# Kernel optimization log

Measured on AMD Instinct MI355X. Metric: run time of the kernel, lower is better.

## Reference

```python
import jax, jax.numpy as jnp
import numpy as np

BLOCKS = (1, 2, 3, 4)      # (block_size, offset=0) from max_block_size=4
BLOCK_MULT = 12            # lcm(1,2,3,4)
DS = 4                     # downsample_factor
MAX_BS = 4                 # max block size (also pos_conv kernel size)
DIM = 512
VOCAB = 256


def _masked_mean(t, m, axis):
    # t: [..., L, D], m: [..., L] bool -> mean over axis with mask, 0 where empty
    mf = m[..., None].astype(t.dtype)
    num = jnp.sum(t * mf, axis=axis)
    tot = jnp.sum(mf, axis=axis)
    mean = num / jnp.clip(tot, 1.0)
    return jnp.where(tot == 0.0, jnp.zeros_like(mean), mean)


def setup_inputs() -> dict:
    key = jax.random.key(0)
    ks = jax.random.split(key, 8)
    B, S = 8, 2048
    return {
        "x": jax.random.randint(ks[0], (B, S), 0, VOCAB),
        "mask": jnp.ones((B, S), dtype=bool),
        "emb": jax.random.normal(ks[1], (VOCAB, DIM), jnp.float32) * 0.02,
        "dw_w": jax.random.normal(ks[2], (MAX_BS, 1, DIM), jnp.float32) * 0.1,   # depthwise kernel (W, I=1, O=DIM)
        "dw_b": jnp.zeros((DIM,), jnp.float32),
        "pw_w": jax.random.normal(ks[3], (1, DIM, DIM), jnp.float32) * 0.03,     # pointwise 1x1 conv
        "pw_b": jnp.zeros((DIM,), jnp.float32),
        "score_w": jax.random.normal(ks[4], (DIM, 1), jnp.float32) * 0.05,
        "score_b": jnp.zeros((1,), jnp.float32),
    }


def reference(x, mask, emb, dw_w, dw_b, pw_w, pw_b, score_w, score_b):
    B, S = x.shape
    D = DIM
    trunc = ((S + DS - 1) // DS) * DS  # next_divisible_length(S, DS); equals S here

    h = emb[x]                                              # [B,S,D]
    h = jnp.pad(h, ((0, 0), (0, MAX_BS - 1), (0, 0)))       # right pad for VALID conv
    dn = jax.lax.conv_dimension_numbers(h.shape, dw_w.shape, ('NWC', 'WIO', 'NWC'))
    h = jax.lax.conv_general_dilated(h, dw_w, (1,), 'VALID',
                                     dimension_numbers=dn,
                                     feature_group_count=D) + dw_b  # depthwise -> [B,S,D]
    h = jnp.einsum('bsd,de->bse', h, pw_w[0]) + pw_b                # pointwise

    # pad seq to multiple of lcm of block sizes
    Sp = ((h.shape[1] + BLOCK_MULT - 1) // BLOCK_MULT) * BLOCK_MULT
    pad = Sp - h.shape[1]
    h = jnp.pad(h, ((0, 0), (0, pad), (0, 0)))
    m = jnp.pad(mask.astype(bool), ((0, 0), (0, pad)), constant_values=False)

    reprs, rmasks = [], []
    for bsz in BLOCKS:  # fixed small set of block sizes (offset=0 for all)
        nb = Sp // bsz
        g = h.reshape(B, nb, bsz, D)
        mg = m.reshape(B, nb, bsz)
        r = _masked_mean(g, mg, axis=2)                       # [B,nb,D]
        reprs.append(jnp.repeat(r, bsz, axis=1))              # [B,Sp,D]
        rmasks.append(jnp.repeat(jnp.any(mg, axis=-1), bsz, axis=1))

    block_reprs = jnp.stack(reprs, axis=2)    # [B,Sp,M,D]
    block_masks = jnp.stack(rmasks, axis=2)   # [B,Sp,M]

    scores = (block_reprs @ score_w)[..., 0] + score_b[0]     # [B,Sp,M]
    max_neg = -jnp.finfo(scores.dtype).max
    scores = jnp.where(block_masks, scores, max_neg)
    scores = jnp.nan_to_num(jax.nn.softmax(scores, axis=2), nan=0.0)

    # consensus attention over positions
    sim = jnp.einsum('bim,bjm->bij', scores, scores)          # [B,Sp,Sp]
    cm = m[:, :, None] & m[:, None, :]
    sim = jnp.where(cm, sim, max_neg)
    attn = jnp.nan_to_num(jax.nn.softmax(sim, axis=-1), nan=0.0)
    scores = jnp.einsum('bij,bjm->bim', attn, scores)

    out = jnp.einsum('bsmd,bsm->bsd', block_reprs, scores)    # weighted combine
    out = out[:, :trunc]
    mt = m[:, :trunc]

    nl = trunc // DS
    xb = out.reshape(B, nl, DS, D)
    mb = mt.reshape(B, nl, DS)
    out = _masked_mean(xb, mb, axis=2)                        # [B, S/DS, D]
    out_mask = jnp.any(mb, axis=-1)
    return out, out_mask
```

## Files before the change

### kernel.cpp

```cpp
#include <hip/hip_runtime.h>
#include <stdint.h>
#include <stddef.h>

typedef __bf16 bf16_t;
typedef bf16_t bf16x4v __attribute__((ext_vector_type(4)));
typedef bf16_t bf16x8v __attribute__((ext_vector_type(8)));
typedef float  f32x4   __attribute__((ext_vector_type(4)));

#define NBATCH 8
#define SEQ    2048
#define DIM    512
#define SP     2052
#define NL     512

static __device__ __forceinline__ f32x4 ldbf4(const bf16_t* p) {
  bf16x4v v = *(const bf16x4v*)p;
  f32x4 r;
  r.x = (float)v[0]; r.y = (float)v[1]; r.z = (float)v[2]; r.w = (float)v[3];
  return r;
}
static __device__ __forceinline__ void stbf4(bf16_t* p, f32x4 v) {
  bf16x4v o;
  o[0] = (bf16_t)v.x; o[1] = (bf16_t)v.y; o[2] = (bf16_t)v.z; o[3] = (bf16_t)v.w;
  *(bf16x4v*)p = o;
}

static __device__ __forceinline__ void gload_lds16(const void* g, void* l) {
  __builtin_amdgcn_global_load_lds(
      (const __attribute__((address_space(1))) void*)g,
      (__attribute__((address_space(3))) void*)l, 16, 0, 0);
}

#define GA_WT   256
#define GA_MASK 65
#define GA_A    (NBATCH * SEQ / 2)
__global__ __launch_bounds__(256) void kA_prep(
    const float* __restrict__ pw, bf16_t* __restrict__ Wt,
    const void* __restrict__ mraw, float* __restrict__ mask01,
    const int* __restrict__ x, const float* __restrict__ emb,
    const float* __restrict__ dww, const float* __restrict__ dwb,
    bf16_t* __restrict__ A) {
  const int bx = blockIdx.x, t = threadIdx.x;
  if (bx < GA_WT) {
    __shared__ float T[32][33];
    int ti = bx >> 4, tj = bx & 15;
    int r = t >> 3, c0 = (t & 7) * 4;
    f32x4 v = *(const f32x4*)(pw + (size_t)(ti * 32 + r) * DIM + tj * 32 + c0);
    T[c0 + 0][r] = v.x; T[c0 + 1][r] = v.y;
    T[c0 + 2][r] = v.z; T[c0 + 3][r] = v.w;
    __syncthreads();
    bf16x4v o;
    o[0] = (bf16_t)T[r][c0 + 0]; o[1] = (bf16_t)T[r][c0 + 1];
    o[2] = (bf16_t)T[r][c0 + 2]; o[3] = (bf16_t)T[r][c0 + 3];
    *(bf16x4v*)(Wt + (size_t)(tj * 32 + r) * DIM + ti * 32 + c0) = o;
    return;
  }
  if (bx < GA_WT + GA_MASK) {
    int idx = (bx - GA_WT) * 256 + t;
    if (idx >= NBATCH * SP) return;
    int b = idx / SP, s = idx - b * SP;
    const unsigned char* mb = (const unsigned char*)mraw;
    int u8 = 0;
#pragma unroll
    for (int i = 0; i < 64; i++)
      if ((i & 3) != 0 && mb[i] != 0) u8 = 1;
    float v = 0.f;
    if (s < SEQ) {
      int mi = b * SEQ + s;
      int nz = u8 ? (mb[mi] != 0) : (((const int*)mraw)[mi] != 0);
      v = nz ? 1.f : 0.f;
    }
    mask01[idx] = v;
    return;
  }
  int rp = bx - (GA_WT + GA_MASK);
  int row = rp * 2 + (t >> 7);
  int b = row >> 11, s = row & 2047;
  int d0 = (t & 127) * 4;
  f32x4 acc = *(const f32x4*)(dwb + d0);
#pragma unroll
  for (int tt = 0; tt < 4; tt++) {
    int sp = s + tt;
    if (sp < SEQ) {
      int v = x[b * SEQ + sp];
      f32x4 e = *(const f32x4*)(emb + (size_t)v * DIM + d0);
      f32x4 w = *(const f32x4*)(dww + tt * DIM + d0);
      acc += e * w;
    }
  }
  stbf4(A + (size_t)row * DIM + d0, acc);
}

#define BM 64
#define BN 128
#define BK 32
__global__ __launch_bounds__(256) void k2_gemm(
    const bf16_t* __restrict__ A, const bf16_t* __restrict__ Bt,
    const float* __restrict__ bias, bf16_t* __restrict__ H) {
  __shared__ __align__(16) bf16_t As[BM * BK];
  __shared__ __align__(16) bf16_t Bs[BN * BK];
  const int t = threadIdx.x;
  const int bid = blockIdx.x;
  const int xcd = bid & 7, loc = bid >> 3;
  const int mt = xcd * 32 + (loc >> 2);
  const int nt = loc & 3;
  const int m0 = mt * BM, n0 = nt * BN;
  const int lane = t & 63, wave = t >> 6;
  const int wm = (wave & 1) * 32, wn = (wave >> 1) * 64;
  const int mloc = lane & 15, quad = lane >> 4;

  f32x4 acc[2][4] = {};

  char* asd  = (char*)As + t * 16;
  char* bsd1 = (char*)Bs + t * 16;
  char* bsd2 = (char*)Bs + (t + 256) * 16;
  const int ar = t >> 2,           ak = (t & 3) * 8;
  const int br1 = t >> 2,          bk1 = (t & 3) * 8;
  const int br2 = (t + 256) >> 2,  bk2 = (t & 3) * 8;

  for (int k0 = 0; k0 < 512; k0 += BK) {
    gload_lds16(A + (size_t)(m0 + ar) * DIM + k0 + ak, asd);
    gload_lds16(Bt + (size_t)(n0 + br1) * DIM + k0 + bk1, bsd1);
    gload_lds16(Bt + (size_t)(n0 + br2) * DIM + k0 + bk2, bsd2);
    __syncthreads();
    bf16x8v af[2], bfr[4];
#pragma unroll
    for (int i = 0; i < 2; i++)
      af[i] = *(const bf16x8v*)&As[(wm + i * 16 + mloc) * BK + quad * 8];
#pragma unroll
    for (int i = 0; i < 4; i++)
      bfr[i] = *(const bf16x8v*)&Bs[(wn + i * 16 + mloc) * BK + quad * 8];
#pragma unroll
    for (int mi = 0; mi < 2; mi++)
#pragma unroll
      for (int ni = 0; ni < 4; ni++)
        acc[mi][ni] = __builtin_amdgcn_mfma_f32_16x16x32_bf16(
            af[mi], bfr[ni], acc[mi][ni], 0, 0, 0);
    __syncthreads();
  }
#pragma unroll
  for (int ni = 0; ni < 4; ni++) {
    int col = n0 + wn + ni * 16 + mloc;
    float bv = bias[col];
#pragma unroll
    for (int mi = 0; mi < 2; mi++) {
      int rbase = m0 + wm + mi * 16 + quad * 4;
#pragma unroll
      for (int r = 0; r < 4; r++)
        H[(size_t)(rbase + r) * DIM + col] = (bf16_t)(acc[mi][ni][r] + bv);
    }
  }
}

__global__ __launch_bounds__(128) void kB_p(
    const bf16_t* __restrict__ H, const float* __restrict__ mask01,
    const float* __restrict__ sw, const float* __restrict__ sbp,
    float* __restrict__ P) {
  const int b = blockIdx.x, c = blockIdx.y;
  const int s0 = c * 12;
  const int t = threadIdx.x;
  const int d0 = t * 4;
  const float sb = sbp[0];

  float ms[12], p[12];
  f32x4 swv = *(const f32x4*)(sw + d0);
#pragma unroll
  for (int i = 0; i < 12; i++) {
    int s = s0 + i;
    ms[i] = mask01[b * SP + s];
    if (s < SEQ) {
      f32x4 h = ldbf4(H + ((size_t)b * SEQ + s) * DIM + d0);
      p[i] = h.x * swv.x + h.y * swv.y + h.z * swv.z + h.w * swv.w;
    } else {
      p[i] = 0.f;
    }
  }
#pragma unroll
  for (int off = 32; off > 0; off >>= 1)
#pragma unroll
    for (int i = 0; i < 12; i++) p[i] += __shfl_down(p[i], off);
  __shared__ float hsw[2][12];
  int lane = t & 63, wv = t >> 6;
  if (lane == 0)
#pragma unroll
    for (int i = 0; i < 12; i++) hsw[wv][i] = p[i];
  __syncthreads();
#define HSUM(i) (hsw[0][i] + hsw[1][i])
  if (t < 12) {
    int i = t;
    float m1 = ms[i];
    float v1 = HSUM(i) * m1 + sb;
    int i2 = i & ~1;
    float cc2 = ms[i2] + ms[i2 + 1];
    float s2 = HSUM(i2) * ms[i2] + HSUM(i2 + 1) * ms[i2 + 1];
    float v2 = (cc2 > 0.f ? s2 / cc2 : 0.f) + sb;
    int i3 = (i >= 9) ? 9 : (i >= 6) ? 6 : (i >= 3) ? 3 : 0;
    float cc3 = ms[i3] + ms[i3 + 1] + ms[i3 + 2];
    float s3 = HSUM(i3) * ms[i3] + HSUM(i3 + 1) * ms[i3 + 1] +
               HSUM(i3 + 2) * ms[i3 + 2];
    float v3 = (cc3 > 0.f ? s3 / cc3 : 0.f) + sb;
    int i4 = i & ~3;
    float cc4 = ms[i4] + ms[i4 + 1] + ms[i4 + 2] + ms[i4 + 3];
    float s4 = HSUM(i4) * ms[i4] + HSUM(i4 + 1) * ms[i4 + 1] +
               HSUM(i4 + 2) * ms[i4 + 2] + HSUM(i4 + 3) * ms[i4 + 3];
    float v4 = (cc4 > 0.f ? s4 / cc4 : 0.f) + sb;
    const float NEG = -3.0e38f;
    float a1 = m1 > 0.f ? v1 : NEG, a2 = cc2 > 0.f ? v2 : NEG;
    float a3 = cc3 > 0.f ? v3 : NEG, a4 = cc4 > 0.f ? v4 : NEG;
    float mx = fmaxf(fmaxf(a1, a2), fmaxf(a3, a4));
    f32x4 o;
    if (mx <= NEG) {
      o.x = o.y = o.z = o.w = 0.25f;
    } else {
      float e1 = m1 > 0.f ? __expf(v1 - mx) : 0.f;
      float e2 = cc2 > 0.f ? __expf(v2 - mx) : 0.f;
      float e3 = cc3 > 0.f ? __expf(v3 - mx) : 0.f;
      float e4 = cc4 > 0.f ? __expf(v4 - mx) : 0.f;
      float inv = 1.f / (e1 + e2 + e3 + e4);
      o.x = e1 * inv; o.y = e2 * inv; o.z = e3 * inv; o.w = e4 * inv;
    }
    *(f32x4*)(P + ((size_t)b * SP + s0 + i) * 4) = o;
  }
#undef HSUM
}

#define KS  16
#define KJL 129
__global__ __launch_bounds__(256) void k56_out(
    const bf16_t* __restrict__ H, const float* __restrict__ P,
    const float* __restrict__ mask01, float* __restrict__ out,
    float* __restrict__ omask) {
  const int b = blockIdx.x, yb = blockIdx.y;
  const int t = threadIdx.x;
  const int S0 = yb * KS;
  __shared__ f32x4 Q[SP];
  __shared__ f32x4 wsh[KS];
  __shared__ float msh[KS + 8];
  __shared__ float red[4];

  float cnt0 = 0.f;
  for (int j = t; j < SP; j += 256) {
    f32x4 q = *(const f32x4*)(P + ((size_t)b * SP + j) * 4);
    if (mask01[b * SP + j] == 0.f) {
      q.x = q.y = q.z = q.w = 0.f;
      cnt0 += 1.f;
    }
    Q[j] = q;
  }
  if (t < KS + 8) {
    int s = S0 - 2 + t;
    msh[t] = (s >= 0 && s < SP) ? mask01[b * SP + s] : 0.f;
  }
#pragma unroll
  for (int off = 32; off > 0; off >>= 1) cnt0 += __shfl_down(cnt0, off);
  if ((t & 63) == 0) red[t >> 6] = cnt0;
  __syncthreads();
  const float nmask = red[0] + red[1] + red[2] + red[3];

  {
    const int il = t >> 4, jc = t & 15;
    const f32x4 qi = Q[S0 + il];
    int j0 = jc * KJL, j1 = j0 + KJL;
    if (j1 > SP) j1 = SP;
    f32x4 acc; acc.x = acc.y = acc.z = acc.w = 0.f;
    float den = 0.f;
    for (int j = j0; j < j1; j++) {
      f32x4 pj = Q[j];
      float sim = qi.x * pj.x + qi.y * pj.y + qi.z * pj.z + qi.w * pj.w;
      float e = __expf(sim);
      den += e;
      acc += e * pj;
    }
#pragma unroll
    for (int off = 8; off > 0; off >>= 1) {
      acc.x += __shfl_down(acc.x, off); acc.y += __shfl_down(acc.y, off);
      acc.z += __shfl_down(acc.z, off); acc.w += __shfl_down(acc.w, off);
      den += __shfl_down(den, off);
    }
    if (jc == 0) {
      den -= nmask;
      float inv = den > 0.f ? 1.f / den : 0.f;
      f32x4 w;
      w.x = acc.x * inv; w.y = acc.y * inv;
      w.z = acc.z * inv; w.w = acc.w * inv;
      wsh[il] = w;
    }
  }
  __syncthreads();

#pragma unroll
  for (int it = 0; it < 2; it++) {
    const int slot = it * 256 + t;
    const int ll = slot >> 7;
    const int d0 = (slot & 127) * 4;
    const int sb = ll * 4;
    f32x4 h[8]; float mk[8];
#pragma unroll
    for (int k = 0; k < 8; k++) {
      mk[k] = msh[sb + k];
      int sg = S0 + sb - 2 + k;
      sg = sg < 0 ? 0 : (sg > SEQ - 1 ? SEQ - 1 : sg);
      h[k] = ldbf4(H + ((size_t)b * SEQ + sg) * DIM + d0);
    }
    float c4 = mk[2] + mk[3] + mk[4] + mk[5];
    float i4 = c4 > 0.f ? 1.f / c4 : 0.f;
    f32x4 r4 = (h[2] * mk[2] + h[3] * mk[3] + h[4] * mk[4] + h[5] * mk[5]) * i4;
    float c2a = mk[2] + mk[3], c2b = mk[4] + mk[5];
    f32x4 r2a = (h[2] * mk[2] + h[3] * mk[3]) * (c2a > 0.f ? 1.f / c2a : 0.f);
    f32x4 r2b = (h[4] * mk[4] + h[5] * mk[5]) * (c2b > 0.f ? 1.f / c2b : 0.f);
    const f32x4 w0 = wsh[sb], w1 = wsh[sb + 1];
    const f32x4 w2 = wsh[sb + 2], w3 = wsh[sb + 3];
#define MEAN3(K)                                                         \
    ((h[K] * mk[K] + h[(K) + 1] * mk[(K) + 1] + h[(K) + 2] * mk[(K) + 2]) * \
     ((mk[K] + mk[(K) + 1] + mk[(K) + 2]) > 0.f                          \
          ? 1.f / (mk[K] + mk[(K) + 1] + mk[(K) + 2]) : 0.f))
    f32x4 o;
    const int r = (S0 + sb) % 3;
    if (r == 0) {
      f32x4 A = MEAN3(2), B = MEAN3(5);
      o = mk[2] * (w0.x * h[2] + w0.y * r2a + w0.z * A + w0.w * r4)
        + mk[3] * (w1.x * h[3] + w1.y * r2a + w1.z * A + w1.w * r4)
        + mk[4] * (w2.x * h[4] + w2.y * r2b + w2.z * A + w2.w * r4)
        + mk[5] * (w3.x * h[5] + w3.y * r2b + w3.z * B + w3.w * r4);
    } else if (r == 1) {
      f32x4 A = MEAN3(1), B = MEAN3(4);
      o = mk[2] * (w0.x * h[2] + w0.y * r2a + w0.z * A + w0.w * r4)
        + mk[3] * (w1.x * h[3] + w1.y * r2a + w1.z * A + w1.w * r4)
        + mk[4] * (w2.x * h[4] + w2.y * r2b + w2.z * B + w2.w * r4)
        + mk[5] * (w3.x * h[5] + w3.y * r2b + w3.z * B + w3.w * r4);
    } else {
      f32x4 A = MEAN3(0), B = MEAN3(3);
      o = mk[2] * (w0.x * h[2] + w0.y * r2a + w0.z * A + w0.w * r4)
        + mk[3] * (w1.x * h[3] + w1.y * r2a + w1.z * B + w1.w * r4)
        + mk[4] * (w2.x * h[4] + w2.y * r2b + w2.z * B + w2.w * r4)
        + mk[5] * (w3.x * h[5] + w3.y * r2b + w3.z * B + w3.w * r4);
    }
#undef MEAN3
    o *= i4;
    const int l = yb * 4 + ll;
    *(f32x4*)(out + ((size_t)b * NL + l) * DIM + d0) = o;
    if (d0 == 0) omask[b * NL + l] = c4 > 0.f ? 1.f : 0.f;
  }
}

extern "C" void kernel_launch(void* const* d_in, const int* in_sizes, int n_in,
                              void* d_out, int out_size, void* d_ws, size_t ws_size,
                              hipStream_t stream) {
  const int*   x    = (const int*)d_in[0];
  const void*  mraw = d_in[1];
  const float* emb  = (const float*)d_in[2];
  const float* dww  = (const float*)d_in[3];
  const float* dwb  = (const float*)d_in[4];
  const float* pw   = (const float*)d_in[5];
  const float* pwb  = (const float*)d_in[6];
  const float* sw   = (const float*)d_in[7];
  const float* sb   = (const float*)d_in[8];

  char* ws = (char*)d_ws;
  size_t off = 0;
  auto alloc = [&](size_t bytes) {
    size_t o = off;
    off = (off + bytes + 255) & ~(size_t)255;
    return o;
  };
  bf16_t* A     = (bf16_t*)(ws + alloc((size_t)NBATCH * SEQ * DIM * 2));
  bf16_t* H     = (bf16_t*)(ws + alloc((size_t)NBATCH * SEQ * DIM * 2));
  bf16_t* Wt    = (bf16_t*)(ws + alloc((size_t)DIM * DIM * 2));
  float* mask01 = (float*)(ws + alloc((size_t)NBATCH * SP * 4));
  float* P      = (float*)(ws + alloc((size_t)NBATCH * SP * 4 * 4));

  float* out   = (float*)d_out;
  float* omask = out + (size_t)NBATCH * NL * DIM;

  kA_prep<<<GA_WT + GA_MASK + GA_A, 256, 0, stream>>>(pw, Wt, mraw, mask01,
                                                      x, emb, dww, dwb, A);
  k2_gemm<<<1024, 256, 0, stream>>>(A, Wt, pwb, H);
  kB_p<<<dim3(NBATCH, 171), 128, 0, stream>>>(H, mask01, sw, sb, P);
  k56_out<<<dim3(NBATCH, 128), 256, 0, stream>>>(H, P, mask01, out, omask);
}
```

Before: 143.9 us.

## Precompute per-token pointwise projections as lookup table instead of full GEMM

Because the depthwise conv followed by a linear pointwise projection is linear in the embeddings, the code projects each (tap, vocab) pair once. It builds a 1088x512 table of emb*dw_w rows plus the bias, multiplies it by the pointwise weights in a small GEMM, then forms each H row by summing four gathered table rows plus the bias. This removes the 16384x512x512 GEMM and the intermediate A buffer. In exchange the score kernel now performs four fp32 row gathers per position, and the summation runs in fp32 with different rounding from the previous bf16 GEMM path.

After: 131.6 us. -8.5%, faster.

```diff
diff --git a/kernel.cpp b/kernel.cpp
--- a/kernel.cpp
+++ b/kernel.cpp
@@ -12,6 +12,7 @@
 #define DIM    512
 #define SP     2052
 #define NL     512
+#define MROWS  1088
 
 static __device__ __forceinline__ f32x4 ldbf4(const bf16_t* p) {
   bf16x4v v = *(const bf16x4v*)p;
@@ -31,17 +32,16 @@
       (__attribute__((address_space(3))) void*)l, 16, 0, 0);
 }
 
-#define GA_WT   256
-#define GA_MASK 65
-#define GA_A    (NBATCH * SEQ / 2)
-__global__ __launch_bounds__(256) void kA_prep(
+#define GP_WT   256
+#define GP_MASK 65
+#define GP_SC   544
+__global__ __launch_bounds__(256) void kP_prep(
     const float* __restrict__ pw, bf16_t* __restrict__ Wt,
     const void* __restrict__ mraw, float* __restrict__ mask01,
-    const int* __restrict__ x, const float* __restrict__ emb,
-    const float* __restrict__ dww, const float* __restrict__ dwb,
-    bf16_t* __restrict__ A) {
+    const float* __restrict__ emb, const float* __restrict__ dww,
+    const float* __restrict__ dwb, bf16_t* __restrict__ At) {
   const int bx = blockIdx.x, t = threadIdx.x;
-  if (bx < GA_WT) {
+  if (bx < GP_WT) {
     __shared__ float T[32][33];
     int ti = bx >> 4, tj = bx & 15;
     int r = t >> 3, c0 = (t & 7) * 4;
@@ -55,8 +55,8 @@
     *(bf16x4v*)(Wt + (size_t)(tj * 32 + r) * DIM + ti * 32 + c0) = o;
     return;
   }
-  if (bx < GA_WT + GA_MASK) {
-    int idx = (bx - GA_WT) * 256 + t;
+  if (bx < GP_WT + GP_MASK) {
+    int idx = (bx - GP_WT) * 256 + t;
     if (idx >= NBATCH * SP) return;
     int b = idx / SP, s = idx - b * SP;
     const unsigned char* mb = (const unsigned char*)mraw;
@@ -73,37 +73,33 @@
     mask01[idx] = v;
     return;
   }
-  int rp = bx - (GA_WT + GA_MASK);
-  int row = rp * 2 + (t >> 7);
-  int b = row >> 11, s = row & 2047;
-  int d0 = (t & 127) * 4;
-  f32x4 acc = *(const f32x4*)(dwb + d0);
-#pragma unroll
-  for (int tt = 0; tt < 4; tt++) {
-    int sp = s + tt;
-    if (sp < SEQ) {
-      int v = x[b * SEQ + sp];
-      f32x4 e = *(const f32x4*)(emb + (size_t)v * DIM + d0);
-      f32x4 w = *(const f32x4*)(dww + tt * DIM + d0);
-      acc += e * w;
-    }
-  }
-  stbf4(A + (size_t)row * DIM + d0, acc);
+  int idx = (bx - (GP_WT + GP_MASK)) * 256 + t;
+  int r = idx >> 7, d0 = (idx & 127) * 4;
+  f32x4 o4;
+  if (r < 1024) {
+    int tt = r >> 8, v = r & 255;
+    f32x4 e = *(const f32x4*)(emb + (size_t)v * DIM + d0);
+    f32x4 w = *(const f32x4*)(dww + tt * DIM + d0);
+    o4 = e * w;
+  } else if (r == 1024) {
+    o4 = *(const f32x4*)(dwb + d0);
+  } else {
+    o4.x = o4.y = o4.z = o4.w = 0.f;
+  }
+  stbf4(At + (size_t)r * DIM + d0, o4);
 }
 
 #define BM 64
 #define BN 128
 #define BK 32
-__global__ __launch_bounds__(256) void k2_gemm(
+__global__ __launch_bounds__(256) void kM_gemm(
     const bf16_t* __restrict__ A, const bf16_t* __restrict__ Bt,
-    const float* __restrict__ bias, bf16_t* __restrict__ H) {
+    float* __restrict__ M) {
   __shared__ __align__(16) bf16_t As[BM * BK];
   __shared__ __align__(16) bf16_t Bs[BN * BK];
   const int t = threadIdx.x;
-  const int bid = blockIdx.x;
-  const int xcd = bid & 7, loc = bid >> 3;
-  const int mt = xcd * 32 + (loc >> 2);
-  const int nt = loc & 3;
+  const int mt = blockIdx.x >> 2;
+  const int nt = blockIdx.x & 3;
   const int m0 = mt * BM, n0 = nt * BN;
   const int lane = t & 63, wave = t >> 6;
   const int wm = (wave & 1) * 32, wn = (wave >> 1) * 64;
@@ -141,36 +137,47 @@
 #pragma unroll
   for (int ni = 0; ni < 4; ni++) {
     int col = n0 + wn + ni * 16 + mloc;
-    float bv = bias[col];
 #pragma unroll
     for (int mi = 0; mi < 2; mi++) {
       int rbase = m0 + wm + mi * 16 + quad * 4;
 #pragma unroll
       for (int r = 0; r < 4; r++)
-        H[(size_t)(rbase + r) * DIM + col] = (bf16_t)(acc[mi][ni][r] + bv);
-    }
-  }
-}
-
-__global__ __launch_bounds__(128) void kB_p(
-    const bf16_t* __restrict__ H, const float* __restrict__ mask01,
+        M[(size_t)(rbase + r) * DIM + col] = acc[mi][ni][r];
+    }
+  }
+}
+
+__global__ __launch_bounds__(128) void kB_hp(
+    const float* __restrict__ Mt, const int* __restrict__ x,
+    const float* __restrict__ pwb, const float* __restrict__ mask01,
     const float* __restrict__ sw, const float* __restrict__ sbp,
-    float* __restrict__ P) {
+    bf16_t* __restrict__ H, float* __restrict__ P) {
   const int b = blockIdx.x, c = blockIdx.y;
   const int s0 = c * 12;
   const int t = threadIdx.x;
   const int d0 = t * 4;
   const float sb = sbp[0];
 
+  f32x4 swv = *(const f32x4*)(sw + d0);
+  f32x4 bias2 = *(const f32x4*)(Mt + (size_t)1024 * DIM + d0)
+              + *(const f32x4*)(pwb + d0);
   float ms[12], p[12];
-  f32x4 swv = *(const f32x4*)(sw + d0);
 #pragma unroll
   for (int i = 0; i < 12; i++) {
     int s = s0 + i;
     ms[i] = mask01[b * SP + s];
     if (s < SEQ) {
-      f32x4 h = ldbf4(H + ((size_t)b * SEQ + s) * DIM + d0);
+      f32x4 h = bias2;
+      int base = b * SEQ + s;
+#pragma unroll
+      for (int tt = 0; tt < 4; tt++) {
+        if (s + tt < SEQ) {
+          int v = x[base + tt];
+          h += *(const f32x4*)(Mt + (size_t)((tt << 8) + v) * DIM + d0);
+        }
+      }
       p[i] = h.x * swv.x + h.y * swv.y + h.z * swv.z + h.w * swv.w;
+      stbf4(H + ((size_t)b * SEQ + s) * DIM + d0, h);
     } else {
       p[i] = 0.f;
     }
@@ -363,18 +370,20 @@
     off = (off + bytes + 255) & ~(size_t)255;
     return o;
   };
-  bf16_t* A     = (bf16_t*)(ws + alloc((size_t)NBATCH * SEQ * DIM * 2));
   bf16_t* H     = (bf16_t*)(ws + alloc((size_t)NBATCH * SEQ * DIM * 2));
   bf16_t* Wt    = (bf16_t*)(ws + alloc((size_t)DIM * DIM * 2));
+  bf16_t* At    = (bf16_t*)(ws + alloc((size_t)MROWS * DIM * 2));
+  float*  Mt    = (float*)(ws + alloc((size_t)MROWS * DIM * 4));
   float* mask01 = (float*)(ws + alloc((size_t)NBATCH * SP * 4));
   float* P      = (float*)(ws + alloc((size_t)NBATCH * SP * 4 * 4));
 
   float* out   = (float*)d_out;
   float* omask = out + (size_t)NBATCH * NL * DIM;
 
-  kA_prep<<<GA_WT + GA_MASK + GA_A, 256, 0, stream>>>(pw, Wt, mraw, mask01,
-                                                      x, emb, dww, dwb, A);
-  k2_gemm<<<1024, 256, 0, stream>>>(A, Wt, pwb, H);
-  kB_p<<<dim3(NBATCH, 171), 128, 0, stream>>>(H, mask01, sw, sb, P);
+  kP_prep<<<GP_WT + GP_MASK + GP_SC, 256, 0, stream>>>(pw, Wt, mraw, mask01,
+                                                       emb, dww, dwb, At);
+  kM_gemm<<<68, 256, 0, stream>>>(At, Wt, Mt);
+  kB_hp<<<dim3(NBATCH, 171), 128, 0, stream>>>(Mt, x, pwb, mask01, sw, sb,
+                                               H, P);
   k56_out<<<dim3(NBATCH, 128), 256, 0, stream>>>(H, P, mask01, out, omask);
 }
```
